# Optimization experiments

Measured on AMD Instinct MI355X. Metric: run time of the kernel, lower is better.

The kernel has to match this reference:

```python
import jax, jax.numpy as jnp
import numpy as np
import math

EMBED_DIMS = 256
NUM_HEADS = 8
NUM_LEVELS = 4
NUM_POINTS = 8
SPATIAL_SHAPES = np.array([[92, 160], [46, 80], [23, 40], [12, 20]], dtype=np.int32)


def _offset_bias():
    # Faithful to reset_parameters(): per-head unit directions scaled by point index.
    thetas = np.arange(NUM_HEADS, dtype=np.float32) * (2.0 * math.pi / NUM_HEADS)
    grid = np.stack([np.cos(thetas), np.sin(thetas)], axis=-1)
    grid = grid / np.abs(grid).max(axis=-1, keepdims=True)
    grid = np.tile(grid[:, None, None, :], (1, NUM_LEVELS, NUM_POINTS, 1))
    for i in range(NUM_POINTS):
        grid[:, :, i, :] *= i + 1
    return grid.reshape(-1).astype(np.float32)


def setup_inputs() -> dict:
    key = jax.random.key(0)
    ks = jax.random.split(key, 8)
    B, Q, E = 4, 10000, EMBED_DIMS
    S = int((SPATIAL_SHAPES[:, 0] * SPATIAL_SHAPES[:, 1]).sum())
    Z = 4  # num_z_anchors; NUM_POINTS % Z == 0
    query = jax.random.normal(ks[0], (B, Q, E), dtype=jnp.float32)
    value = jax.random.normal(ks[1], (B, S, E), dtype=jnp.float32)
    reference_points = jax.random.uniform(ks[2], (B, Q, Z, 2), dtype=jnp.float32)
    # Learned params (random weights so the math is fully exercised; bias per original init).
    w_off = jax.random.normal(ks[3], (E, NUM_HEADS * NUM_LEVELS * NUM_POINTS * 2), dtype=jnp.float32) * 0.01
    b_off = jnp.asarray(_offset_bias())
    w_attn = jax.random.normal(ks[4], (E, NUM_HEADS * NUM_LEVELS * NUM_POINTS), dtype=jnp.float32) * 0.02
    b_attn = jnp.zeros((NUM_HEADS * NUM_LEVELS * NUM_POINTS,), dtype=jnp.float32)
    w_val = jax.random.normal(ks[5], (E, E), dtype=jnp.float32) * (1.0 / np.sqrt(E))
    b_val = jnp.zeros((E,), dtype=jnp.float32)
    return {
        "query": query, "value": value, "reference_points": reference_points,
        "w_off": w_off, "b_off": b_off, "w_attn": w_attn, "b_attn": b_attn,
        "w_val": w_val, "b_val": b_val,
        "spatial_shapes": jnp.asarray(SPATIAL_SHAPES),
    }


def _bilinear_sample(img, px, py):
    """grid_sample(bilinear, padding=zeros, align_corners=False).
    img: [N, H, W, D]; px, py: [N, Q, P] in pixel coords. Returns [N, Q, P, D]."""
    H, W = img.shape[1], img.shape[2]
    x0 = jnp.floor(px); y0 = jnp.floor(py)
    wx = (px - x0)[..., None]; wy = (py - y0)[..., None]
    x0i = x0.astype(jnp.int32); y0i = y0.astype(jnp.int32)
    x1i = x0i + 1; y1i = y0i + 1
    bidx = jnp.arange(img.shape[0])[:, None, None]
    def gather(yy, xx):
        m = ((yy >= 0) & (yy < H) & (xx >= 0) & (xx < W)).astype(img.dtype)[..., None]
        return img[bidx, jnp.clip(yy, 0, H - 1), jnp.clip(xx, 0, W - 1)] * m
    v00 = gather(y0i, x0i); v01 = gather(y0i, x1i)
    v10 = gather(y1i, x0i); v11 = gather(y1i, x1i)
    return (v00 * (1 - wx) + v01 * wx) * (1 - wy) + (v10 * (1 - wx) + v11 * wx) * wy


def _forward(query, value, reference_points, w_off, b_off, w_attn, b_attn, w_val, b_val, shapes_np):
    B, Q, E = query.shape
    NH, L, NP = NUM_HEADS, shapes_np.shape[0], NUM_POINTS
    D = E // NH
    v = (value @ w_val + b_val).reshape(B, -1, NH, D)  # [B, S, NH, D]
    off = (query @ w_off + b_off).reshape(B, Q, NH, L, NP, 2)
    attn = jax.nn.softmax((query @ w_attn + b_attn).reshape(B, Q, NH, L * NP), axis=-1)
    attn = attn.reshape(B, Q, NH, L, NP)
    # Normalize offsets by (W, H) per level.
    norm = jnp.asarray(np.stack([shapes_np[:, 1], shapes_np[:, 0]], axis=-1), dtype=off.dtype)  # [L,2]
    off = off / norm[None, None, None, :, None, :]
    Z = reference_points.shape[2]
    off = off.reshape(B, Q, NH, L, NP // Z, Z, 2)
    loc = reference_points[:, :, None, None, None, :, :] + off  # [B,Q,NH,L,NP/Z,Z,2]
    loc = loc.reshape(B, Q, NH, L, NP, 2)
    out = jnp.zeros((B, Q, NH, D), dtype=query.dtype)
    start = 0
    for lvl in range(L):
        hl, wl = int(shapes_np[lvl, 0]), int(shapes_np[lvl, 1])
        seg = v[:, start:start + hl * wl]
        start += hl * wl
        img = seg.reshape(B, hl, wl, NH, D).transpose(0, 3, 1, 2, 4).reshape(B * NH, hl, wl, D)
        g = loc[:, :, :, lvl].transpose(0, 2, 1, 3, 4).reshape(B * NH, Q, NP, 2)
        # align_corners=False: pixel = norm_coord * size - 0.5
        px = g[..., 0] * wl - 0.5
        py = g[..., 1] * hl - 0.5
        samp = _bilinear_sample(img, px, py)  # [B*NH, Q, NP, D]
        w = attn[:, :, :, lvl].transpose(0, 2, 1, 3).reshape(B * NH, Q, NP)
        out = out + jnp.einsum('nqpd,nqp->nqd', samp, w).reshape(B, NH, Q, D).transpose(0, 2, 1, 3)
    return out.reshape(B, Q, NH * D)


def reference(query, value, reference_points, w_off, b_off, w_attn, b_attn, w_val, b_val, spatial_shapes):
    shapes_np = np.asarray(spatial_shapes)
    return _forward(query, value, reference_points, w_off, b_off, w_attn, b_attn, w_val, b_val, shapes_np)
```

## Files before the change

### kernel.cpp

```cpp
#include <hip/hip_runtime.h>

#define BATCH    4
#define NQ       10000
#define EMB      256
#define NH       8
#define DH       32
#define NL       4
#define NP       8
#define S_TOTAL  19560
#define NROW     (BATCH * NQ)
#define VROWS    (BATCH * S_TOTAL)

typedef _Float16 half8 __attribute__((ext_vector_type(8)));
typedef _Float16 half4v __attribute__((ext_vector_type(4)));
typedef _Float16 half2v __attribute__((ext_vector_type(2)));
typedef float floatx4 __attribute__((ext_vector_type(4)));

__global__ __launch_bounds__(256) void conv_f16(
    const float* __restrict__ in, _Float16* __restrict__ out, size_t total) {
  const size_t e = ((size_t)blockIdx.x * 256 + threadIdx.x) * 8;
  if (e >= total) return;
  const float4 f0 = *(const float4*)(in + e);
  const float4 f1 = *(const float4*)(in + e + 4);
  half8 h;
  h[0] = (_Float16)f0.x; h[1] = (_Float16)f0.y;
  h[2] = (_Float16)f0.z; h[3] = (_Float16)f0.w;
  h[4] = (_Float16)f1.x; h[5] = (_Float16)f1.y;
  h[6] = (_Float16)f1.z; h[7] = (_Float16)f1.w;
  *(half8*)(out + e) = h;
}

__global__ __launch_bounds__(256) void transp_f16(
    const float* __restrict__ W, _Float16* __restrict__ WT, int N) {
  const int tid = blockIdx.x * 256 + threadIdx.x;
  const int n = tid >> 8, k = tid & 255;
  WT[(size_t)n * 256 + k] = (_Float16)W[(size_t)k * N + n];
}

__global__ __launch_bounds__(256) void bias_cat(
    const float* __restrict__ b0, const float* __restrict__ b1,
    float* __restrict__ o) {
  const int t = blockIdx.x * 256 + threadIdx.x;
  if (t < 512) o[t] = b0[t];
  else if (t < 768) o[t] = b1[t - 512];
}

template <int NC, bool SWZ>
__global__ __launch_bounds__(256, 2) void gemm2(
    const _Float16* __restrict__ A, const _Float16* __restrict__ WT,
    const float* __restrict__ bias, _Float16* __restrict__ C, int M) {
  __shared__ _Float16 bs[128 * 264];
  const int t = threadIdx.x;
  const int wave = t >> 6, lane = t & 63;
  const int l15 = lane & 15, quad = lane >> 4;
  const int m0 = blockIdx.x * 256 + wave * 64;
  const int n0 = blockIdx.y * 128;

  #pragma unroll
  for (int j = 0; j < 16; ++j) {
    const int c = t + 256 * j;
    const int n = c >> 5, ck = c & 31;
    *(half8*)&bs[n * 264 + ck * 8] =
        *(const half8*)(WT + (size_t)(n0 + n) * 256 + ck * 8);
  }

  const _Float16* Ab[4];
  #pragma unroll
  for (int i = 0; i < 4; ++i) {
    const int row = min(m0 + 16 * i + l15, M - 1);
    Ab[i] = A + (size_t)row * 256 + quad * 8;
  }
  float bcol[8];
  #pragma unroll
  for (int j = 0; j < 8; ++j) bcol[j] = bias[n0 + 16 * j + l15];

  floatx4 acc[4][8] = {};
  half8 ring[2][4];
  #pragma unroll
  for (int i = 0; i < 4; ++i) ring[0][i] = *(const half8*)(Ab[i]);
  #pragma unroll
  for (int i = 0; i < 4; ++i) ring[1][i] = *(const half8*)(Ab[i] + 32);

  __syncthreads();

  const int koff = quad * 8;
  #pragma unroll
  for (int ks = 0; ks < 8; ++ks) {
    half8 cur[4];
    #pragma unroll
    for (int i = 0; i < 4; ++i) cur[i] = ring[ks & 1][i];
    if (ks < 6) {
      #pragma unroll
      for (int i = 0; i < 4; ++i)
        ring[ks & 1][i] = *(const half8*)(Ab[i] + (ks + 2) * 32);
    }
    #pragma unroll
    for (int j = 0; j < 8; ++j) {
      const half8 b = *(const half8*)&bs[(16 * j + l15) * 264 + ks * 32 + koff];
      #pragma unroll
      for (int i = 0; i < 4; ++i)
        acc[i][j] = __builtin_amdgcn_mfma_f32_16x16x32_f16(cur[i], b, acc[i][j], 0, 0, 0);
    }
  }

  #pragma unroll
  for (int i = 0; i < 4; ++i) {
    #pragma unroll
    for (int r = 0; r < 4; ++r) {
      const int row = m0 + 16 * i + quad * 4 + r;
      if (row < M) {
        if (SWZ) {
          const int b = row / S_TOTAL;
          const int s = row - b * S_TOTAL;
          #pragma unroll
          for (int j = 0; j < 8; ++j) {
            const int col = n0 + 16 * j + l15;
            const size_t dst =
                (((size_t)b * NH + (col >> 5)) * S_TOTAL + s) * 32 + (col & 31);
            C[dst] = (_Float16)(acc[i][j][r] + bcol[j]);
          }
        } else {
          #pragma unroll
          for (int j = 0; j < 8; ++j)
            C[(size_t)row * NC + n0 + 16 * j + l15] =
                (_Float16)(acc[i][j][r] + bcol[j]);
        }
      }
    }
  }
}

__global__ __launch_bounds__(256) void msda_sample(
    const _Float16* __restrict__ vproj,
    const _Float16* __restrict__ fused,
    const float* __restrict__ ref,
    float* __restrict__ out) {
  const int lvl_h[NL] = {92, 46, 23, 12};
  const int lvl_w[NL] = {160, 80, 40, 20};
  const int lvl_s[NL] = {0, 14720, 18400, 19320};

  __shared__ int   addr_s[512];
  __shared__ float wl_s[512];
  __shared__ float wr_s[512];

  const int t   = threadIdx.x;
  const int blk = blockIdx.x;
  const int b   = blk & 3;
  const int q   = blk >> 2;
  const int row = b * NQ + q;

  const int h  = t >> 5;
  const int lp = t & 31;
  const int l  = lp >> 3;
  const int p  = lp & 7;

  const float logit = (float)fused[(size_t)row * 768 + 512 + t];
  float mxv = logit;
  #pragma unroll
  for (int m = 1; m < 32; m <<= 1) mxv = fmaxf(mxv, __shfl_xor(mxv, m));
  const float e = __expf(logit - mxv);
  float sum = e;
  #pragma unroll
  for (int m = 1; m < 32; m <<= 1) sum += __shfl_xor(sum, m);
  const float attnw = e / sum;

  const half2v o2 = *(const half2v*)(fused + (size_t)row * 768 + 2 * t);
  const float ox = (float)o2[0], oy = (float)o2[1];
  const int z = p & 3;
  const float rx = ref[((size_t)row * 4 + z) * 2 + 0];
  const float ry = ref[((size_t)row * 4 + z) * 2 + 1];
  const int Wl = lvl_w[l], Hl = lvl_h[l], st = lvl_s[l];

  const float px = fmaf(rx, (float)Wl, ox) - 0.5f;
  const float py = fmaf(ry, (float)Hl, oy) - 0.5f;
  const float x0f = floorf(px), y0f = floorf(py);
  const float wx = px - x0f, wy = py - y0f;
  const int x0 = (int)x0f, y0 = (int)y0f;
  const int x1 = x0 + 1,   y1 = y0 + 1;

  const float mx0 = (x0 >= 0 && x0 < Wl) ? 1.f : 0.f;
  const float mx1 = (x1 >= 0 && x1 < Wl) ? 1.f : 0.f;
  const float my0 = (y0 >= 0 && y0 < Hl) ? 1.f : 0.f;
  const float my1 = (y1 >= 0 && y1 < Hl) ? 1.f : 0.f;
  const int xb  = min(max(x0, -1), Wl - 1);
  const int cy0 = min(max(y0, 0), Hl - 1);
  const int cy1 = min(max(y1, 0), Hl - 1);

  const int bh   = b * NH + h;
  const int lbase = bh * S_TOTAL + st;
  const float wlc = attnw * (1.f - wx) * mx0;
  const float wrc = attnw * wx * mx1;

  addr_s[2 * t + 0] = (lbase + cy0 * Wl + xb) * 32;
  addr_s[2 * t + 1] = (lbase + cy1 * Wl + xb) * 32;
  wl_s[2 * t + 0] = wlc * (1.f - wy) * my0;
  wr_s[2 * t + 0] = wrc * (1.f - wy) * my0;
  wl_s[2 * t + 1] = wlc * wy * my1;
  wr_s[2 * t + 1] = wrc * wy * my1;
  __syncthreads();

  const int g  = t & 31;
  const int c  = g & 7;
  const int sd = (g >> 3) & 1;
  const int ph = g >> 4;
  const int ldoff = sd * 32 + 4 * c;

  float a0 = 0.f, a1 = 0.f, a2 = 0.f, a3 = 0.f;
  #pragma unroll 8
  for (int i = 0; i < 16; ++i) {
    const int idx = ((h << 5) + 2 * i + ph) * 2;
    const int at = addr_s[idx],     ab = addr_s[idx + 1];
    const float wt = sd ? wr_s[idx]     : wl_s[idx];
    const float wb = sd ? wr_s[idx + 1] : wl_s[idx + 1];
    const half4v vt = *(const half4v*)(vproj + at + ldoff);
    const half4v vb = *(const half4v*)(vproj + ab + ldoff);
    a0 = fmaf(wt, (float)vt[0], a0); a1 = fmaf(wt, (float)vt[1], a1);
    a2 = fmaf(wt, (float)vt[2], a2); a3 = fmaf(wt, (float)vt[3], a3);
    a0 = fmaf(wb, (float)vb[0], a0); a1 = fmaf(wb, (float)vb[1], a1);
    a2 = fmaf(wb, (float)vb[2], a2); a3 = fmaf(wb, (float)vb[3], a3);
  }

  a0 += __shfl_xor(a0, 8);  a1 += __shfl_xor(a1, 8);
  a2 += __shfl_xor(a2, 8);  a3 += __shfl_xor(a3, 8);
  a0 += __shfl_xor(a0, 16); a1 += __shfl_xor(a1, 16);
  a2 += __shfl_xor(a2, 16); a3 += __shfl_xor(a3, 16);

  if (g < 8) {
    float4 o; o.x = a0; o.y = a1; o.z = a2; o.w = a3;
    *(float4*)(out + (size_t)row * 256 + (h << 5) + 4 * c) = o;
  }
}

extern "C" void kernel_launch(void* const* d_in, const int* in_sizes, int n_in,
                              void* d_out, int out_size, void* d_ws, size_t ws_size,
                              hipStream_t stream) {
  const float* query  = (const float*)d_in[0];
  const float* value  = (const float*)d_in[1];
  const float* refpts = (const float*)d_in[2];
  const float* w_off  = (const float*)d_in[3];
  const float* b_off  = (const float*)d_in[4];
  const float* w_attn = (const float*)d_in[5];
  const float* b_attn = (const float*)d_in[6];
  const float* w_val  = (const float*)d_in[7];
  const float* b_val  = (const float*)d_in[8];
  float* out = (float*)d_out;

  char* p = (char*)d_ws;
  _Float16* qh    = (_Float16*)p;  p += (size_t)NROW * 256 * 2;
  _Float16* vah   = (_Float16*)p;  p += (size_t)VROWS * 256 * 2;
  p += 256;
  _Float16* vh    = (_Float16*)p;  p += (size_t)VROWS * 256 * 2;
  p += 256;
  _Float16* wT768 = (_Float16*)p;  p += (size_t)768 * 256 * 2;
  _Float16* wvaT  = (_Float16*)p;  p += (size_t)256 * 256 * 2;
  float*    bias768 = (float*)p;   p += 768 * 4;
  _Float16* fused_h = (_Float16*)p; p += (size_t)NROW * 768 * 2;

  conv_f16<<<(NROW * 256 / 8 + 255) / 256, 256, 0, stream>>>(
      query, qh, (size_t)NROW * 256);
  conv_f16<<<(VROWS * 256 / 8 + 255) / 256, 256, 0, stream>>>(
      value, vah, (size_t)VROWS * 256);
  transp_f16<<<512, 256, 0, stream>>>(w_off, wT768, 512);
  transp_f16<<<256, 256, 0, stream>>>(w_attn, wT768 + 512 * 256, 256);
  transp_f16<<<256, 256, 0, stream>>>(w_val, wvaT, 256);
  bias_cat<<<3, 256, 0, stream>>>(b_off, b_attn, bias768);

  gemm2<256, true><<<dim3((VROWS + 255) / 256, 2), 256, 0, stream>>>(
      vah, wvaT, b_val, vh, VROWS);
  gemm2<768, false><<<dim3((NROW + 255) / 256, 6), 256, 0, stream>>>(
      qh, wT768, bias768, fused_h, NROW);

  msda_sample<<<dim3(NROW), 256, 0, stream>>>(vh, fused_h, refpts, out);
}
```

Before: 466.7 us.

## Fuse fp32-to-fp16 conversion into GEMMs and keep A tile in registers

Drops the separate fp32-to-fp16 conversion kernels for query and value. The GEMM now reads fp32 rows directly, converts them to fp16 in registers, and holds the whole K=256 A fragment in registers. It then loops over N in chunks of 64, streaming B straight from global memory with no LDS staging. This removes a full read/write round trip of the activations and two launches. The cost is many more registers per thread and B reads that are not shared through LDS, which may lower occupancy and raise L2 traffic.

```diff
diff --git a/kernel.cpp b/kernel.cpp
--- a/kernel.cpp
+++ b/kernel.cpp
@@ -16,20 +16,6 @@
 typedef _Float16 half2v __attribute__((ext_vector_type(2)));
 typedef float floatx4 __attribute__((ext_vector_type(4)));
 
-__global__ __launch_bounds__(256) void conv_f16(
-    const float* __restrict__ in, _Float16* __restrict__ out, size_t total) {
-  const size_t e = ((size_t)blockIdx.x * 256 + threadIdx.x) * 8;
-  if (e >= total) return;
-  const float4 f0 = *(const float4*)(in + e);
-  const float4 f1 = *(const float4*)(in + e + 4);
-  half8 h;
-  h[0] = (_Float16)f0.x; h[1] = (_Float16)f0.y;
-  h[2] = (_Float16)f0.z; h[3] = (_Float16)f0.w;
-  h[4] = (_Float16)f1.x; h[5] = (_Float16)f1.y;
-  h[6] = (_Float16)f1.z; h[7] = (_Float16)f1.w;
-  *(half8*)(out + e) = h;
-}
-
 __global__ __launch_bounds__(256) void transp_f16(
     const float* __restrict__ W, _Float16* __restrict__ WT, int N) {
   const int tid = blockIdx.x * 256 + threadIdx.x;
@@ -45,85 +31,91 @@
   else if (t < 768) o[t] = b1[t - 512];
 }
 
-template <int NC, bool SWZ>
-__global__ __launch_bounds__(256, 2) void gemm2(
-    const _Float16* __restrict__ A, const _Float16* __restrict__ WT,
+template <int NC, int NYS, bool SWZ>
+__global__ __launch_bounds__(256, 2) void gemm3(
+    const float* __restrict__ A, const _Float16* __restrict__ WT,
     const float* __restrict__ bias, _Float16* __restrict__ C, int M) {
-  __shared__ _Float16 bs[128 * 264];
   const int t = threadIdx.x;
   const int wave = t >> 6, lane = t & 63;
   const int l15 = lane & 15, quad = lane >> 4;
-  const int m0 = blockIdx.x * 256 + wave * 64;
-  const int n0 = blockIdx.y * 128;
-
-  #pragma unroll
-  for (int j = 0; j < 16; ++j) {
-    const int c = t + 256 * j;
-    const int n = c >> 5, ck = c & 31;
-    *(half8*)&bs[n * 264 + ck * 8] =
-        *(const half8*)(WT + (size_t)(n0 + n) * 256 + ck * 8);
-  }
-
-  const _Float16* Ab[4];
-  #pragma unroll
-  for (int i = 0; i < 4; ++i) {
-    const int row = min(m0 + 16 * i + l15, M - 1);
-    Ab[i] = A + (size_t)row * 256 + quad * 8;
-  }
-  float bcol[8];
-  #pragma unroll
-  for (int j = 0; j < 8; ++j) bcol[j] = bias[n0 + 16 * j + l15];
-
-  floatx4 acc[4][8] = {};
-  half8 ring[2][4];
-  #pragma unroll
-  for (int i = 0; i < 4; ++i) ring[0][i] = *(const half8*)(Ab[i]);
-  #pragma unroll
-  for (int i = 0; i < 4; ++i) ring[1][i] = *(const half8*)(Ab[i] + 32);
-
-  __syncthreads();
-
-  const int koff = quad * 8;
-  #pragma unroll
-  for (int ks = 0; ks < 8; ++ks) {
-    half8 cur[4];
-    #pragma unroll
-    for (int i = 0; i < 4; ++i) cur[i] = ring[ks & 1][i];
-    if (ks < 6) {
+  const int m0 = blockIdx.x * 128 + wave * 32;
+  const int nlo = blockIdx.y * (NC / NYS);
+  const int nhi = nlo + (NC / NYS);
+
+  const float* Arow[2];
+  #pragma unroll
+  for (int i = 0; i < 2; ++i)
+    Arow[i] = A + (size_t)min(m0 + 16 * i + l15, M - 1) * 256 + quad * 8;
+
+  half8 a[2][8];
+  #pragma unroll
+  for (int i = 0; i < 2; ++i) {
+    float4 tmp[8][2];
+    #pragma unroll
+    for (int ks = 0; ks < 8; ++ks) {
+      tmp[ks][0] = *(const float4*)(Arow[i] + ks * 32);
+      tmp[ks][1] = *(const float4*)(Arow[i] + ks * 32 + 4);
+    }
+    #pragma unroll
+    for (int ks = 0; ks < 8; ++ks) {
+      a[i][ks][0] = (_Float16)tmp[ks][0].x; a[i][ks][1] = (_Float16)tmp[ks][0].y;
+      a[i][ks][2] = (_Float16)tmp[ks][0].z; a[i][ks][3] = (_Float16)tmp[ks][0].w;
+      a[i][ks][4] = (_Float16)tmp[ks][1].x; a[i][ks][5] = (_Float16)tmp[ks][1].y;
+      a[i][ks][6] = (_Float16)tmp[ks][1].z; a[i][ks][7] = (_Float16)tmp[ks][1].w;
+    }
+  }
+
+  const _Float16* Bb = WT + (size_t)l15 * 256 + quad * 8;
+
+  for (int n0 = nlo; n0 < nhi; n0 += 64) {
+    float bc[4];
+    #pragma unroll
+    for (int j = 0; j < 4; ++j) bc[j] = bias[n0 + 16 * j + l15];
+
+    floatx4 acc[2][4] = {};
+    half8 bcur[4], bnxt[4];
+    #pragma unroll
+    for (int j = 0; j < 4; ++j)
+      bcur[j] = *(const half8*)(Bb + (size_t)(n0 + 16 * j) * 256);
+
+    #pragma unroll
+    for (int ks = 0; ks < 8; ++ks) {
+      if (ks < 7) {
+        #pragma unroll
+        for (int j = 0; j < 4; ++j)
+          bnxt[j] = *(const half8*)(Bb + (size_t)(n0 + 16 * j) * 256 + (ks + 1) * 32);
+      }
       #pragma unroll
-      for (int i = 0; i < 4; ++i)
-        ring[ks & 1][i] = *(const half8*)(Ab[i] + (ks + 2) * 32);
-    }
-    #pragma unroll
-    for (int j = 0; j < 8; ++j) {
-      const half8 b = *(const half8*)&bs[(16 * j + l15) * 264 + ks * 32 + koff];
+      for (int j = 0; j < 4; ++j)
+        #pragma unroll
+        for (int i = 0; i < 2; ++i)
+          acc[i][j] = __builtin_amdgcn_mfma_f32_16x16x32_f16(a[i][ks], bcur[j], acc[i][j], 0, 0, 0);
       #pragma unroll
-      for (int i = 0; i < 4; ++i)
-        acc[i][j] = __builtin_amdgcn_mfma_f32_16x16x32_f16(cur[i], b, acc[i][j], 0, 0, 0);
-    }
-  }
-
-  #pragma unroll
-  for (int i = 0; i < 4; ++i) {
-    #pragma unroll
-    for (int r = 0; r < 4; ++r) {
-      const int row = m0 + 16 * i + quad * 4 + r;
-      if (row < M) {
-        if (SWZ) {
-          const int b = row / S_TOTAL;
-          const int s = row - b * S_TOTAL;
-          #pragma unroll
-          for (int j = 0; j < 8; ++j) {
-            const int col = n0 + 16 * j + l15;
-            const size_t dst =
-                (((size_t)b * NH + (col >> 5)) * S_TOTAL + s) * 32 + (col & 31);
-            C[dst] = (_Float16)(acc[i][j][r] + bcol[j]);
+      for (int j = 0; j < 4; ++j) bcur[j] = bnxt[j];
+    }
+
+    #pragma unroll
+    for (int i = 0; i < 2; ++i) {
+      #pragma unroll
+      for (int r = 0; r < 4; ++r) {
+        const int row = m0 + 16 * i + quad * 4 + r;
+        if (row < M) {
+          if (SWZ) {
+            const int b = row / S_TOTAL;
+            const int s = row - b * S_TOTAL;
+            #pragma unroll
+            for (int j = 0; j < 4; ++j) {
+              const int col = n0 + 16 * j + l15;
+              const size_t dst =
+                  (((size_t)b * NH + (col >> 5)) * S_TOTAL + s) * 32 + (col & 31);
+              C[dst] = (_Float16)(acc[i][j][r] + bc[j]);
+            }
+          } else {
+            #pragma unroll
+            for (int j = 0; j < 4; ++j)
+              C[(size_t)row * NC + n0 + 16 * j + l15] =
+                  (_Float16)(acc[i][j][r] + bc[j]);
           }
-        } else {
-          #pragma unroll
-          for (int j = 0; j < 8; ++j)
-            C[(size_t)row * NC + n0 + 16 * j + l15] =
-                (_Float16)(acc[i][j][r] + bcol[j]);
         }
       }
     }
@@ -246,8 +238,6 @@
   float* out = (float*)d_out;
 
   char* p = (char*)d_ws;
-  _Float16* qh    = (_Float16*)p;  p += (size_t)NROW * 256 * 2;
-  _Float16* vah   = (_Float16*)p;  p += (size_t)VROWS * 256 * 2;
   p += 256;
   _Float16* vh    = (_Float16*)p;  p += (size_t)VROWS * 256 * 2;
   p += 256;
@@ -256,19 +246,15 @@
   float*    bias768 = (float*)p;   p += 768 * 4;
   _Float16* fused_h = (_Float16*)p; p += (size_t)NROW * 768 * 2;
 
-  conv_f16<<<(NROW * 256 / 8 + 255) / 256, 256, 0, stream>>>(
-      query, qh, (size_t)NROW * 256);
-  conv_f16<<<(VROWS * 256 / 8 + 255) / 256, 256, 0, stream>>>(
-      value, vah, (size_t)VROWS * 256);
   transp_f16<<<512, 256, 0, stream>>>(w_off, wT768, 512);
   transp_f16<<<256, 256, 0, stream>>>(w_attn, wT768 + 512 * 256, 256);
   transp_f16<<<256, 256, 0, stream>>>(w_val, wvaT, 256);
   bias_cat<<<3, 256, 0, stream>>>(b_off, b_attn, bias768);
 
-  gemm2<256, true><<<dim3((VROWS + 255) / 256, 2), 256, 0, stream>>>(
-      vah, wvaT, b_val, vh, VROWS);
-  gemm2<768, false><<<dim3((NROW + 255) / 256, 6), 256, 0, stream>>>(
-      qh, wT768, bias768, fused_h, NROW);
+  gemm3<256, 1, true><<<dim3((VROWS + 127) / 128, 1), 256, 0, stream>>>(
+      value, wvaT, b_val, vh, VROWS);
+  gemm3<768, 2, false><<<dim3((NROW + 127) / 128, 2), 256, 0, stream>>>(
+      query, wT768, bias768, fused_h, NROW);
 
   msda_sample<<<dim3(NROW), 256, 0, stream>>>(vh, fused_h, refpts, out);
 }
```

Measured after the change: 525.2 us. 1.13x slower.
